# Optimization experiments

Measured on AMD Instinct MI355X. Metric: run time of the kernel, lower is better.

Reference implementation:

```python
import jax, jax.numpy as jnp
import numpy as np

B, H, N, D = 2, 16, 2048, 64
SPARSE_TOPK = 64


def setup_inputs() -> dict:
    key = jax.random.key(0)
    ks = jax.random.split(key, 6)
    return {
        "q": jax.random.normal(ks[0], (B, H, N, D), dtype=jnp.float32),
        "k": jax.random.normal(ks[1], (B, H, N, D), dtype=jnp.float32),
        "v": jax.random.normal(ks[2], (B, H, N, D), dtype=jnp.float32),
        "attn_bias": jax.random.normal(ks[3], (H, N, N), dtype=jnp.float32),
        "w_pre": jax.random.normal(ks[4], (H, H), dtype=jnp.float32) * (1.0 / H ** 0.5),
        "w_post": jax.random.normal(ks[5], (H, H), dtype=jnp.float32) * (1.0 / H ** 0.5),
        "sparse_topk": SPARSE_TOPK,
    }


def reference(q, k, v, attn_bias, w_pre, w_post, sparse_topk):
    scale = q.shape[-1] ** -0.5
    # QK^T similarities  [b, h, i, j]
    dots = jnp.einsum('bhid,bhjd->bhij', q, k) * scale
    # pre-softmax talking heads (1x1 conv over head dim)
    dots = jnp.einsum('gh,bhij->bgij', w_pre, dots)
    # attention bias, per head
    dots = dots + attn_bias[None]
    mask_value = -jnp.finfo(dots.dtype).max
    # sparse top-k masking (faithful to source: keep entries strictly below
    # the k-th largest value, i.e. sparse_topk_mask = dots < top_values[..., -1:])
    top_values = jax.lax.top_k(dots, sparse_topk)[0]  # [b,h,i,k]
    kth = top_values[..., -1:]
    keep = dots < kth
    dots = jnp.where(keep, dots, mask_value)
    # softmax computed in float32 (attn_fn = partial(F.softmax, dtype=float32))
    attn = jax.nn.softmax(dots.astype(jnp.float32), axis=-1).astype(q.dtype)
    # post-softmax talking heads
    attn = jnp.einsum('gh,bhij->bgij', w_post, attn)
    # AV
    out = jnp.einsum('bhij,bhjd->bhid', attn, v)
    return out
```

## Files before the change

kernel.cpp:

```cpp
#include <hip/hip_runtime.h>
#include <hip/hip_fp16.h>

#define B_ 2
#define H_ 16
#define N_ 2048
#define D_ 64

typedef __attribute__((ext_vector_type(8))) __bf16 bf16x8;
typedef __attribute__((ext_vector_type(4))) float f32x4;

__device__ __forceinline__ unsigned short f2bf_rn(float x) {
  unsigned u = __float_as_uint(x);
  unsigned r = (u + 0x7fffu + ((u >> 16) & 1u)) >> 16;
  return (unsigned short)r;
}
__device__ __forceinline__ float bf2f(unsigned short s) {
  return __uint_as_float(((unsigned)s) << 16);
}

__global__ __launch_bounds__(256) void qk_mfma(
    const float* __restrict__ q, const float* __restrict__ k,
    float* __restrict__ S, int bb, int i0, int SI) {
  const int h  = blockIdx.z;
  const int it = blockIdx.y * 64;
  const int jt = blockIdx.x * 64;
  __shared__ unsigned short q1s[64][72], q2s[64][72];
  __shared__ unsigned short k1s[64][72], k2s[64][72];
  const int t = threadIdx.x;
  const float* qb = q + (((size_t)bb * H_ + h) * N_ + (size_t)(i0 + it)) * D_;
  const float* kb = k + (((size_t)bb * H_ + h) * N_ + (size_t)jt) * D_;
#pragma unroll
  for (int l = 0; l < 4; ++l) {
    int e4 = t + l * 256;
    int row = e4 >> 4, c4 = e4 & 15;
    float4 xq = *(const float4*)(qb + (size_t)row * D_ + c4 * 4);
    float4 xk = *(const float4*)(kb + (size_t)row * D_ + c4 * 4);
    float qa[4] = {xq.x, xq.y, xq.z, xq.w};
    float ka[4] = {xk.x, xk.y, xk.z, xk.w};
#pragma unroll
    for (int m = 0; m < 4; ++m) {
      unsigned short h1 = f2bf_rn(qa[m]);
      unsigned short h2 = f2bf_rn(qa[m] - bf2f(h1));
      q1s[row][c4 * 4 + m] = h1;
      q2s[row][c4 * 4 + m] = h2;
      unsigned short g1 = f2bf_rn(ka[m]);
      unsigned short g2 = f2bf_rn(ka[m] - bf2f(g1));
      k1s[row][c4 * 4 + m] = g1;
      k2s[row][c4 * 4 + m] = g2;
    }
  }
  __syncthreads();
  const int lane = t & 63, wv = t >> 6;
  const int lr = lane & 15;
  const int lk = (lane >> 4) * 8;
  const int arow = wv * 16 + lr;
  f32x4 acc[4];
#pragma unroll
  for (int ct = 0; ct < 4; ++ct) acc[ct] = (f32x4){0.f, 0.f, 0.f, 0.f};
#pragma unroll
  for (int ks = 0; ks < 2; ++ks) {
    bf16x8 a1 = *(const bf16x8*)&q1s[arow][ks * 32 + lk];
    bf16x8 a2 = *(const bf16x8*)&q2s[arow][ks * 32 + lk];
#pragma unroll
    for (int ct = 0; ct < 4; ++ct) {
      bf16x8 b1 = *(const bf16x8*)&k1s[ct * 16 + lr][ks * 32 + lk];
      bf16x8 b2 = *(const bf16x8*)&k2s[ct * 16 + lr][ks * 32 + lk];
      acc[ct] = __builtin_amdgcn_mfma_f32_16x16x32_bf16(a1, b1, acc[ct], 0, 0, 0);
      acc[ct] = __builtin_amdgcn_mfma_f32_16x16x32_bf16(a1, b2, acc[ct], 0, 0, 0);
      acc[ct] = __builtin_amdgcn_mfma_f32_16x16x32_bf16(a2, b1, acc[ct], 0, 0, 0);
    }
  }
#pragma unroll
  for (int ct = 0; ct < 4; ++ct)
#pragma unroll
    for (int r = 0; r < 4; ++r) {
      int row = it + wv * 16 + (lane >> 4) * 4 + r;
      int col = jt + ct * 16 + lr;
      S[((size_t)h * SI + row) * N_ + col] = acc[ct][r] * 0.125f;
    }
}

__device__ inline float waveReduceSum(float x) {
#pragma unroll
  for (int off = 32; off > 0; off >>= 1) x += __shfl_xor(x, off, 64);
  return x;
}

__device__ inline float dec_u(unsigned uu) {
  unsigned bbv = (uu >> 31) ? (uu & 0x7fffffffu) : ~uu;
  return __uint_as_float(bbv);
}

__device__ float np_score(
    const float* __restrict__ qg, const float* __restrict__ kg,
    const float* __restrict__ w_pre, const float* __restrict__ bias,
    int bb, int g, int ig, int j) {
  float T = 0.f;
  for (int h = 0; h < 16; ++h) {
    const float* qr = qg + (((size_t)bb * H_ + h) * N_ + ig) * (size_t)D_;
    const float* kr = kg + (((size_t)bb * H_ + h) * N_ + j) * (size_t)D_;
    float lacc[16];
#pragma unroll
    for (int l = 0; l < 16; ++l) {
      float tt = __fmul_rn(qr[48 + l], kr[48 + l]);
      tt = __fmaf_rn(qr[32 + l], kr[32 + l], tt);
      tt = __fmaf_rn(qr[16 + l], kr[16 + l], tt);
      tt = __fmaf_rn(qr[l], kr[l], tt);
      lacc[l] = tt;
    }
    float u8[8];
#pragma unroll
    for (int l2 = 0; l2 < 8; ++l2) u8[l2] = __fadd_rn(lacc[l2], lacc[l2 + 8]);
    float u4[4];
#pragma unroll
    for (int l2 = 0; l2 < 4; ++l2) u4[l2] = __fadd_rn(u8[l2], u8[l2 + 4]);
    float dot = __fadd_rn(__fadd_rn(u4[0], u4[2]), __fadd_rn(u4[1], u4[3]));
    T = __fmaf_rn(w_pre[g * 16 + h], __fmul_rn(dot, 0.125f), T);
  }
  return __fadd_rn(T, bias[((size_t)g * N_ + ig) * N_ + j]);
}

__global__ __launch_bounds__(256) void mid_kernel(
    const float* __restrict__ S, __half* __restrict__ A,
    const float* __restrict__ bias,
    const float* __restrict__ w_pre,
    const int* __restrict__ topk_p,
    const float* __restrict__ qg, const float* __restrict__ kg,
    int bb, int i0, int SI) {
  const int il = blockIdx.x;
  const int ig = i0 + il;
  const int t = threadIdx.x;
  const int lane = t & 63, wv = t >> 6;
  const int g = blockIdx.y * 4 + wv;
  const int K = *topk_p;
  __shared__ float repv_s[4][32];

  float af[32];
#pragma unroll
  for (int c = 0; c < 32; ++c) af[c] = 0.f;
#pragma unroll 1
  for (int h = 0; h < 16; ++h) {
    const float w = w_pre[g * 16 + h];
    const float* Sr = S + ((size_t)h * SI + il) * N_;
#pragma unroll
    for (int c4 = 0; c4 < 8; ++c4) {
      float4 s4 = *(const float4*)&Sr[lane * 4 + 256 * c4];
      af[c4 * 4 + 0] = __fmaf_rn(w, s4.x, af[c4 * 4 + 0]);
      af[c4 * 4 + 1] = __fmaf_rn(w, s4.y, af[c4 * 4 + 1]);
      af[c4 * 4 + 2] = __fmaf_rn(w, s4.z, af[c4 * 4 + 2]);
      af[c4 * 4 + 3] = __fmaf_rn(w, s4.w, af[c4 * 4 + 3]);
    }
  }
  unsigned u[32];
  {
    const float* Br = bias + ((size_t)g * N_ + ig) * N_;
#pragma unroll
    for (int c4 = 0; c4 < 8; ++c4) {
      float4 bv = *(const float4*)&Br[lane * 4 + 256 * c4];
      float x0 = __fadd_rn(af[c4 * 4 + 0], bv.x);
      float x1 = __fadd_rn(af[c4 * 4 + 1], bv.y);
      float x2 = __fadd_rn(af[c4 * 4 + 2], bv.z);
      float x3 = __fadd_rn(af[c4 * 4 + 3], bv.w);
      unsigned b0 = __float_as_uint(x0), b1 = __float_as_uint(x1);
      unsigned b2 = __float_as_uint(x2), b3 = __float_as_uint(x3);
      u[c4 * 4 + 0] = (b0 >> 31) ? ~b0 : (b0 | 0x80000000u);
      u[c4 * 4 + 1] = (b1 >> 31) ? ~b1 : (b1 | 0x80000000u);
      u[c4 * 4 + 2] = (b2 >> 31) ? ~b2 : (b2 | 0x80000000u);
      u[c4 * 4 + 3] = (b3 >> 31) ? ~b3 : (b3 | 0x80000000u);
    }
  }

  unsigned lo = 0u;
  for (int bit = 31; bit >= 0; --bit) {
    unsigned cand = lo | (1u << bit);
    int cnt = 0;
#pragma unroll
    for (int c = 0; c < 32; ++c)
      cnt += (int)__popcll(__ballot(u[c] >= cand));
    if (cnt >= K) lo = cand;
  }
  const float t64 = dec_u(lo);

  const float eps = 4e-3f;
  const float bhi = t64 + eps, blo = t64 - eps;
  int cnt_above = 0, cnt_band = 0;
#pragma unroll
  for (int c = 0; c < 32; ++c) {
    float f = dec_u(u[c]);
    cnt_above += (int)__popcll(__ballot(f > bhi));
    cnt_band  += (int)__popcll(__ballot(f <= bhi && f >= blo));
  }
  const int m = K - cnt_above;
  const bool refined = (cnt_band > m);
  int nm = 0;
  float kth = 3.4e38f;
  if (refined) {
    int myj = 0;
    for (int c = 0; c < 32 && nm < 32; ++c) {
      float f = dec_u(u[c]);
      unsigned long long ba = __ballot(f <= bhi && f >= blo);
      while (ba && nm < 32) {
        int src = __builtin_ctzll(ba); ba &= ba - 1ull;
        int j = src * 4 + 256 * (c >> 2) + (c & 3);
        if (nm == lane) myj = j;
        ++nm;
      }
    }
    float myval = -3.4e38f;
    if (lane < nm) myval = np_score(qg, kg, w_pre, bias, bb, g, ig, myj);
    if (lane < 32) repv_s[wv][lane] = (lane < nm) ? myval : -3.4e38f;
    unsigned chosen = 0;
    for (int s = 0; s < m && s < nm; ++s) {
      float best = -3.4e38f; int bi = -1;
      for (int i2 = 0; i2 < nm; ++i2) {
        if ((chosen >> i2) & 1u) continue;
        float bv = repv_s[wv][i2];
        if (bv > best) { best = bv; bi = i2; }
      }
      if (bi < 0) break;
      chosen |= (1u << bi);
      kth = best;
    }
  }

  float ssum = 0.f;
  int ord = 0;
#pragma unroll
  for (int c = 0; c < 32; ++c) {
    float f = dec_u(u[c]);
    float pv;
    if (refined) {
      bool above = f > bhi;
      bool inb = (!above) && (f >= blo);
      unsigned long long ba = __ballot(inb);
      int myord = ord + (int)__popcll(ba & ((1ull << lane) - 1ull));
      ord += (int)__popcll(ba);
      if (above) pv = 0.f;
      else if (inb) {
        if (myord < nm) {
          float val = repv_s[wv][myord];
          pv = (val >= kth) ? 0.f : __expf(val - t64);
        } else pv = 0.f;
      } else pv = __expf(f - t64);
    } else {
      pv = (f >= blo) ? 0.f : __expf(f - t64);
    }
    u[c] = __float_as_uint(pv);
    ssum += pv;
  }
  ssum = waveReduceSum(ssum);
  const float isv = 1.f / ssum;

  __half* Ab = A + ((size_t)g * SI + il) * N_;
#pragma unroll
  for (int c = 0; c < 8; ++c) {
    int j = lane * 4 + 256 * c;
    float p0 = __uint_as_float(u[c * 4 + 0]) * isv;
    float p1 = __uint_as_float(u[c * 4 + 1]) * isv;
    float p2 = __uint_as_float(u[c * 4 + 2]) * isv;
    float p3 = __uint_as_float(u[c * 4 + 3]) * isv;
    *(__half2*)&Ab[j]     = __floats2half2_rn(p0, p1);
    *(__half2*)&Ab[j + 2] = __floats2half2_rn(p2, p3);
  }
}

__global__ __launch_bounds__(256) void postmixA_kernel(
    const __half* __restrict__ Pn, const float* __restrict__ w_post,
    __half* __restrict__ A2, int SI) {
  const int idx = blockIdx.x * 256 + threadIdx.x;
  const int il = idx >> 10;
  const int jc = (idx & 1023) * 2;
  float2 acc[16];
#pragma unroll
  for (int g = 0; g < 16; ++g) acc[g] = make_float2(0.f, 0.f);
#pragma unroll
  for (int h = 0; h < 16; ++h) {
    __half2 ph = *(const __half2*)&Pn[((size_t)h * SI + il) * N_ + jc];
    float2 pf = __half22float2(ph);
#pragma unroll
    for (int g = 0; g < 16; ++g) {
      const float w = w_post[g * 16 + h];
      acc[g].x = fmaf(w, pf.x, acc[g].x);
      acc[g].y = fmaf(w, pf.y, acc[g].y);
    }
  }
#pragma unroll
  for (int g = 0; g < 16; ++g)
    *(__half2*)&A2[((size_t)g * SI + il) * N_ + jc] =
        __floats2half2_rn(acc[g].x, acc[g].y);
}

__global__ __launch_bounds__(256) void pv_kernel(
    const __half* __restrict__ A, const float* __restrict__ v,
    float* __restrict__ out, int bb, int i0, int SI) {
  const int it = blockIdx.x * 128;
  const int g  = blockIdx.y;
  const int t  = threadIdx.x;
  const int tx = t & 15, ty = t >> 4;
  __shared__ __half as_[128][72];
  __shared__ __half vt[64][72];
  float acc[8][4];
#pragma unroll
  for (int i = 0; i < 8; ++i)
#pragma unroll
    for (int j = 0; j < 4; ++j) acc[i][j] = 0.f;
  const float* vb = v + ((size_t)bb * H_ + g) * (size_t)N_ * D_;

  for (int kb = 0; kb < N_; kb += 64) {
#pragma unroll
    for (int l = 0; l < 4; ++l) {
      int e8 = t + l * 256;
      int row = e8 >> 3, c8 = e8 & 7;
      *(uint4*)&as_[row][c8 * 8] =
          *(const uint4*)&A[((size_t)g * SI + (it + row)) * N_ + kb + c8 * 8];
    }
#pragma unroll
    for (int l = 0; l < 4; ++l) {
      int e4 = t + l * 256;
      int row = e4 >> 4, d4 = e4 & 15;
      float4 x = *(const float4*)&vb[(size_t)(kb + row) * D_ + d4 * 4];
      vt[d4 * 4 + 0][row] = __float2half_rn(x.x);
      vt[d4 * 4 + 1][row] = __float2half_rn(x.y);
      vt[d4 * 4 + 2][row] = __float2half_rn(x.z);
      vt[d4 * 4 + 3][row] = __float2half_rn(x.w);
    }
    __syncthreads();
#pragma unroll
    for (int k8 = 0; k8 < 8; ++k8) {
      float vf[4][8];
#pragma unroll
      for (int dj = 0; dj < 4; ++dj) {
        const __half2* p2 = (const __half2*)&vt[dj * 16 + tx][k8 * 8];
#pragma unroll
        for (int c = 0; c < 4; ++c) {
          float2 f = __half22float2(p2[c]);
          vf[dj][c * 2] = f.x; vf[dj][c * 2 + 1] = f.y;
        }
      }
#pragma unroll
      for (int di = 0; di < 8; ++di) {
        const __half2* a2 = (const __half2*)&as_[di * 16 + ty][k8 * 8];
        float af2[8];
#pragma unroll
        for (int c = 0; c < 4; ++c) {
          float2 f = __half22float2(a2[c]);
          af2[c * 2] = f.x; af2[c * 2 + 1] = f.y;
        }
#pragma unroll
        for (int dj = 0; dj < 4; ++dj)
#pragma unroll
          for (int kk = 0; kk < 8; ++kk)
            acc[di][dj] = fmaf(af2[kk], vf[dj][kk], acc[di][dj]);
      }
    }
    __syncthreads();
  }
  float* ob = out + (((size_t)bb * H_ + g) * N_ + (size_t)(i0 + it)) * D_;
#pragma unroll
  for (int di = 0; di < 8; ++di)
#pragma unroll
    for (int dj = 0; dj < 4; ++dj)
      ob[(size_t)(di * 16 + ty) * D_ + dj * 16 + tx] = acc[di][dj];
}

extern "C" void kernel_launch(void* const* d_in, const int* in_sizes, int n_in,
                              void* d_out, int out_size, void* d_ws, size_t ws_size,
                              hipStream_t stream) {
  const float* q      = (const float*)d_in[0];
  const float* k      = (const float*)d_in[1];
  const float* v      = (const float*)d_in[2];
  const float* bias   = (const float*)d_in[3];
  const float* w_pre  = (const float*)d_in[4];
  const float* w_post = (const float*)d_in[5];
  const int*   topk   = (const int*)d_in[6];
  float* out = (float*)d_out;

  int SI = N_;
  while ((size_t)H_ * SI * N_ * 6 > ws_size && SI > 128) SI >>= 1;
  float*  Sbuf = (float*)d_ws;
  __half* Abuf = (__half*)((char*)d_ws + (size_t)H_ * SI * N_ * 4);
  __half* A2   = (__half*)d_ws;

  for (int b = 0; b < B_; ++b) {
    for (int i0 = 0; i0 < N_; i0 += SI) {
      qk_mfma<<<dim3(N_ / 64, SI / 64, H_), 256, 0, stream>>>(q, k, Sbuf, b, i0, SI);
      mid_kernel<<<dim3(SI, 4), 256, 0, stream>>>(Sbuf, Abuf, bias, w_pre,
                                                  topk, q, k, b, i0, SI);
      postmixA_kernel<<<dim3(SI * (N_ / 2) / 256), 256, 0, stream>>>(Abuf, w_post,
                                                                     A2, SI);
      pv_kernel<<<dim3(SI / 128, H_), 256, 0, stream>>>(A2, v, out, b, i0, SI);
    }
  }
}
```

Baseline: 1.547 ms.

## Use fp16 MFMA for PV matmul and swap mid_kernel grid axes

Replaces the scalar FMA inner loop of the attention-times-V kernel with 16x16x32 fp16 MFMA instructions. Each wave computes a 32x64 output tile from the existing shared-memory fp16 tiles. Separately, mid_kernel's grid is transposed so the four head-group blocks for a row run adjacently, which should improve cache reuse of the S rows they all read. The MFMA path changes the accumulation order, which may alter results slightly.

```diff
diff --git a/kernel.cpp b/kernel.cpp
--- a/kernel.cpp
+++ b/kernel.cpp
@@ -7,6 +7,7 @@
 #define D_ 64
 
 typedef __attribute__((ext_vector_type(8))) __bf16 bf16x8;
+typedef __attribute__((ext_vector_type(8))) _Float16 f16x8;
 typedef __attribute__((ext_vector_type(4))) float f32x4;
 
 __device__ __forceinline__ unsigned short f2bf_rn(float x) {
@@ -127,11 +128,11 @@
     const int* __restrict__ topk_p,
     const float* __restrict__ qg, const float* __restrict__ kg,
     int bb, int i0, int SI) {
-  const int il = blockIdx.x;
+  const int il = blockIdx.y;
   const int ig = i0 + il;
   const int t = threadIdx.x;
   const int lane = t & 63, wv = t >> 6;
-  const int g = blockIdx.y * 4 + wv;
+  const int g = blockIdx.x * 4 + wv;
   const int K = *topk_p;
   __shared__ float repv_s[4][32];
 
@@ -296,14 +297,17 @@
   const int it = blockIdx.x * 128;
   const int g  = blockIdx.y;
   const int t  = threadIdx.x;
-  const int tx = t & 15, ty = t >> 4;
+  const int lane = t & 63, wv = t >> 6;
+  const int lr = lane & 15;
+  const int hi = lane >> 4;
+  const int lk = hi * 8;
   __shared__ __half as_[128][72];
   __shared__ __half vt[64][72];
-  float acc[8][4];
-#pragma unroll
-  for (int i = 0; i < 8; ++i)
-#pragma unroll
-    for (int j = 0; j < 4; ++j) acc[i][j] = 0.f;
+  f32x4 acc[2][4];
+#pragma unroll
+  for (int rt = 0; rt < 2; ++rt)
+#pragma unroll
+    for (int ct = 0; ct < 4; ++ct) acc[rt][ct] = (f32x4){0.f, 0.f, 0.f, 0.f};
   const float* vb = v + ((size_t)bb * H_ + g) * (size_t)N_ * D_;
 
   for (int kb = 0; kb < N_; kb += 64) {
@@ -326,41 +330,27 @@
     }
     __syncthreads();
 #pragma unroll
-    for (int k8 = 0; k8 < 8; ++k8) {
-      float vf[4][8];
-#pragma unroll
-      for (int dj = 0; dj < 4; ++dj) {
-        const __half2* p2 = (const __half2*)&vt[dj * 16 + tx][k8 * 8];
-#pragma unroll
-        for (int c = 0; c < 4; ++c) {
-          float2 f = __half22float2(p2[c]);
-          vf[dj][c * 2] = f.x; vf[dj][c * 2 + 1] = f.y;
-        }
+    for (int ks = 0; ks < 2; ++ks) {
+      f16x8 a0 = *(const f16x8*)&as_[wv * 32 + lr][ks * 32 + lk];
+      f16x8 a1 = *(const f16x8*)&as_[wv * 32 + 16 + lr][ks * 32 + lk];
+#pragma unroll
+      for (int ct = 0; ct < 4; ++ct) {
+        f16x8 bv = *(const f16x8*)&vt[ct * 16 + lr][ks * 32 + lk];
+        acc[0][ct] = __builtin_amdgcn_mfma_f32_16x16x32_f16(a0, bv, acc[0][ct], 0, 0, 0);
+        acc[1][ct] = __builtin_amdgcn_mfma_f32_16x16x32_f16(a1, bv, acc[1][ct], 0, 0, 0);
       }
-#pragma unroll
-      for (int di = 0; di < 8; ++di) {
-        const __half2* a2 = (const __half2*)&as_[di * 16 + ty][k8 * 8];
-        float af2[8];
-#pragma unroll
-        for (int c = 0; c < 4; ++c) {
-          float2 f = __half22float2(a2[c]);
-          af2[c * 2] = f.x; af2[c * 2 + 1] = f.y;
-        }
-#pragma unroll
-        for (int dj = 0; dj < 4; ++dj)
-#pragma unroll
-          for (int kk = 0; kk < 8; ++kk)
-            acc[di][dj] = fmaf(af2[kk], vf[dj][kk], acc[di][dj]);
-      }
     }
     __syncthreads();
   }
   float* ob = out + (((size_t)bb * H_ + g) * N_ + (size_t)(i0 + it)) * D_;
 #pragma unroll
-  for (int di = 0; di < 8; ++di)
-#pragma unroll
-    for (int dj = 0; dj < 4; ++dj)
-      ob[(size_t)(di * 16 + ty) * D_ + dj * 16 + tx] = acc[di][dj];
+  for (int rt = 0; rt < 2; ++rt)
+#pragma unroll
+    for (int ct = 0; ct < 4; ++ct)
+#pragma unroll
+      for (int r = 0; r < 4; ++r)
+        ob[(size_t)(wv * 32 + rt * 16 + hi * 4 + r) * D_ + ct * 16 + lr] =
+            acc[rt][ct][r];
 }
 
 extern "C" void kernel_launch(void* const* d_in, const int* in_sizes, int n_in,
@@ -384,7 +374,7 @@
   for (int b = 0; b < B_; ++b) {
     for (int i0 = 0; i0 < N_; i0 += SI) {
       qk_mfma<<<dim3(N_ / 64, SI / 64, H_), 256, 0, stream>>>(q, k, Sbuf, b, i0, SI);
-      mid_kernel<<<dim3(SI, 4), 256, 0, stream>>>(Sbuf, Abuf, bias, w_pre,
+      mid_kernel<<<dim3(4, SI), 256, 0, stream>>>(Sbuf, Abuf, bias, w_pre,
                                                   topk, q, k, b, i0, SI);
       postmixA_kernel<<<dim3(SI * (N_ / 2) / 256), 256, 0, stream>>>(Abuf, w_post,
                                                                      A2, SI);
```

Result: faster. 1.286 ms (-16.8%).
